# Kernel optimization log

Hardware: AMD Instinct MI355X
Metric: run time of the kernel (lower is better)

Reference implementation:

```python
import jax, jax.numpy as jnp
import numpy as np

N = 50000
E_RAND = 800000
F_IN = 256
F_OUT = 256
ALPHA = 0.2  # LeakyReLU negative slope


def setup_inputs() -> dict:
    key = jax.random.key(0)
    k1, k2, k3, k4 = jax.random.split(key, 4)
    x = jax.random.normal(k1, (N, F_IN), dtype=jnp.float32)
    # random edges + self-loops so every row has at least one edge (avoids div by 0)
    edge_rand = jax.random.randint(k2, (2, E_RAND), 0, N)
    loops = jnp.arange(N)
    edge = jnp.concatenate([edge_rand, jnp.stack([loops, loops])], axis=1)  # [2, 850000]
    W = jax.random.normal(k3, (F_IN, F_OUT), dtype=jnp.float32) * 0.05
    a = jax.random.normal(k4, (2 * F_OUT,), dtype=jnp.float32) * 0.05
    return {"x": x, "edge": edge, "W": W, "a": a}


def reference(x, edge, W, a):
    # x: [N, F_in], edge: [2, E] (row = dst/aggregation index per torch.sparse.mm(a, h))
    n = x.shape[0]
    f_out = W.shape[1]
    h = x @ W  # [N, F_out]
    src, dst = edge[0], edge[1]
    # a @ [h_src; h_dst] decomposes into two per-node dot products (no [E, 2F] concat)
    s = h @ a[:f_out]   # [N]
    t = h @ a[f_out:]   # [N]
    logit = s[src] + t[dst]                                  # [E]
    e = jnp.exp(-jax.nn.leaky_relu(logit, ALPHA))            # [E]
    rowsum = jax.ops.segment_sum(e, src, num_segments=n)     # [N]
    msg = e[:, None] * h[dst]                                # [E, F_out]
    h_prime = jax.ops.segment_sum(msg, src, num_segments=n)  # [N, F_out]
    h_prime = h_prime / rowsum[:, None]
    return jax.nn.relu(h_prime)  # concat=True path
```

## Files before the change

### kernel.cpp

```cpp
#include <hip/hip_runtime.h>
#include <hip/hip_fp16.h>

#define FDIM 256
#define ALPHA 0.2f

typedef _Float16 half8 __attribute__((ext_vector_type(8)));
typedef _Float16 half4 __attribute__((ext_vector_type(4)));
typedef float floatx4 __attribute__((ext_vector_type(4)));

__global__ __launch_bounds__(256) void prep_hist(const float* __restrict__ W,
                                                 _Float16* __restrict__ wswz,
                                                 const int* __restrict__ edge,
                                                 int* __restrict__ deg, int E) {
  if (blockIdx.x < 32) {
    const int g = blockIdx.x * 256 + threadIdx.x;
    const int kc = g >> 11, L = g & 2047;
    const int n = L >> 3, c = L & 7;
    half8 hv;
#pragma unroll
    for (int j = 0; j < 8; ++j)
      hv[j] = (_Float16)W[(size_t)(kc * 64 + c * 8 + j) * 256 + n];
    *(half8*)(wswz + (size_t)g * 8) = hv;
  } else {
    const int e = (blockIdx.x - 32) * 256 + threadIdx.x;
    if (e < E) atomicAdd(&deg[edge[e]], 1);
  }
}

#define HT_STRIDE 264
__global__ __launch_bounds__(256) void gemm_mfma(
    const float* __restrict__ x, const _Float16* __restrict__ wswz,
    const float* __restrict__ a, _Float16* __restrict__ h,
    float* __restrict__ s, float* __restrict__ t, int M) {
  __shared__ __align__(16) _Float16 smem[64 * HT_STRIDE];
  _Float16* As = smem;
  const int tid = threadIdx.x;
  const int w = tid >> 6, l = tid & 63;
  const int l15 = l & 15, q = l >> 4;
  const int row0 = blockIdx.x * 64;

  floatx4 acc[4][4];
#pragma unroll
  for (int mt = 0; mt < 4; ++mt)
#pragma unroll
    for (int nt = 0; nt < 4; ++nt) acc[mt][nt] = (floatx4){0.f, 0.f, 0.f, 0.f};

  const int id0 = tid, id1 = 256 + tid;
  const int m0 = id0 >> 3, c0 = (id0 & 7) ^ (m0 & 7);
  const int m1 = id1 >> 3, c1 = (id1 & 7) ^ (m1 & 7);
  const int r0 = row0 + m0, r1 = row0 + m1;

  float4 pf[2][2];
  auto loadA = [&](int kc) {
    pf[0][0] = pf[0][1] = pf[1][0] = pf[1][1] = make_float4(0.f, 0.f, 0.f, 0.f);
    if (r0 < M) {
      const float4* p = (const float4*)(x + (size_t)r0 * 256 + kc * 64 + c0 * 8);
      pf[0][0] = p[0];
      pf[0][1] = p[1];
    }
    if (r1 < M) {
      const float4* p = (const float4*)(x + (size_t)r1 * 256 + kc * 64 + c1 * 8);
      pf[1][0] = p[0];
      pf[1][1] = p[1];
    }
  };
  auto storeA = [&]() {
#pragma unroll
    for (int hf = 0; hf < 2; ++hf) {
      half8 hv;
      hv[0] = (_Float16)pf[hf][0].x; hv[1] = (_Float16)pf[hf][0].y;
      hv[2] = (_Float16)pf[hf][0].z; hv[3] = (_Float16)pf[hf][0].w;
      hv[4] = (_Float16)pf[hf][1].x; hv[5] = (_Float16)pf[hf][1].y;
      hv[6] = (_Float16)pf[hf][1].z; hv[7] = (_Float16)pf[hf][1].w;
      *(half8*)(As + (size_t)(hf * 256 + tid) * 8) = hv;
    }
  };

  loadA(0);
  for (int kc = 0; kc < 4; ++kc) {
    storeA();
    half8 bf[2][4];
#pragma unroll
    for (int ks = 0; ks < 2; ++ks) {
      const int c = ks * 4 + q;
#pragma unroll
      for (int nt = 0; nt < 4; ++nt) {
        const int n = w * 64 + nt * 16 + l15;
        bf[ks][nt] = *(const half8*)(wswz + (size_t)(kc * 2048 + n * 8 + c) * 8);
      }
    }
    __syncthreads();
    if (kc < 3) loadA(kc + 1);
#pragma unroll
    for (int ks = 0; ks < 2; ++ks) {
      const int c = ks * 4 + q;
      half8 af[4];
#pragma unroll
      for (int mt = 0; mt < 4; ++mt) {
        const int m = mt * 16 + l15;
        af[mt] = *(const half8*)(As + (size_t)(m * 8 + (c ^ (m & 7))) * 8);
      }
#pragma unroll
      for (int mt = 0; mt < 4; ++mt)
#pragma unroll
        for (int nt = 0; nt < 4; ++nt)
          acc[mt][nt] = __builtin_amdgcn_mfma_f32_16x16x32_f16(
              af[mt], bf[ks][nt], acc[mt][nt], 0, 0, 0);
    }
    __syncthreads();
  }

#pragma unroll
  for (int mt = 0; mt < 4; ++mt)
#pragma unroll
    for (int nt = 0; nt < 4; ++nt)
#pragma unroll
      for (int r = 0; r < 4; ++r)
        smem[(size_t)(mt * 16 + q * 4 + r) * HT_STRIDE + w * 64 + nt * 16 +
             l15] = (_Float16)acc[mt][nt][r];
  __syncthreads();

  const int w8 = tid >> 5;
  const int colh = (tid & 31) * 8;
#pragma unroll
  for (int p = 0; p < 8; ++p) {
    const int rl = p * 8 + w8;
    const int row = row0 + rl;
    if (row < M)
      *(half8*)(h + (size_t)row * 256 + colh) =
          *(const half8*)(smem + (size_t)rl * HT_STRIDE + colh);
  }

  const int r8 = tid >> 2, seg = tid & 3;
  float sp = 0.f, tp = 0.f;
#pragma unroll
  for (int c8 = 0; c8 < 8; ++c8) {
    const int col = seg * 64 + c8 * 8;
    const half8 hv = *(const half8*)(smem + (size_t)r8 * HT_STRIDE + col);
    const float4 a0 = *(const float4*)(a + col);
    const float4 a1 = *(const float4*)(a + col + 4);
    const float4 b0 = *(const float4*)(a + 256 + col);
    const float4 b1 = *(const float4*)(a + 256 + col + 4);
    sp += (float)hv[0] * a0.x + (float)hv[1] * a0.y + (float)hv[2] * a0.z +
          (float)hv[3] * a0.w + (float)hv[4] * a1.x + (float)hv[5] * a1.y +
          (float)hv[6] * a1.z + (float)hv[7] * a1.w;
    tp += (float)hv[0] * b0.x + (float)hv[1] * b0.y + (float)hv[2] * b0.z +
          (float)hv[3] * b0.w + (float)hv[4] * b1.x + (float)hv[5] * b1.y +
          (float)hv[6] * b1.z + (float)hv[7] * b1.w;
  }
  sp += __shfl_xor(sp, 1);
  sp += __shfl_xor(sp, 2);
  tp += __shfl_xor(tp, 1);
  tp += __shfl_xor(tp, 2);
  if (seg == 0 && row0 + r8 < M) {
    s[row0 + r8] = sp;
    t[row0 + r8] = tp;
  }
}

__global__ __launch_bounds__(1024) void scan1(const int* __restrict__ deg,
                                              int* __restrict__ rowstart,
                                              int* __restrict__ bsum, int n) {
  const int tid = threadIdx.x;
  const int i = blockIdx.x * 1024 + tid;
  const int val = (i < n) ? deg[i] : 0;
  const int lane = tid & 63, wv = tid >> 6;
  int v = val;
#pragma unroll
  for (int off = 1; off < 64; off <<= 1) {
    const int o = __shfl_up(v, off);
    if (lane >= off) v += o;
  }
  __shared__ int wsum[16];
  __shared__ int woff[16];
  if (lane == 63) wsum[wv] = v;
  __syncthreads();
  if (tid < 16) {
    int wv2 = wsum[tid];
#pragma unroll
    for (int off = 1; off < 16; off <<= 1) {
      const int o = __shfl_up(wv2, off);
      if (tid >= off) wv2 += o;
    }
    woff[tid] = wv2;
  }
  __syncthreads();
  const int incl = v + (wv ? woff[wv - 1] : 0);
  if (i < n) rowstart[i] = incl - val;
  if (tid == 1023) bsum[blockIdx.x] = woff[15];
}

__global__ __launch_bounds__(64) void scan2(const int* __restrict__ bsum,
                                            int* __restrict__ boff,
                                            int* __restrict__ rowstart, int nb,
                                            int n) {
  const int tid = threadIdx.x;
  int v = (tid < nb) ? bsum[tid] : 0;
#pragma unroll
  for (int off = 1; off < 64; off <<= 1) {
    const int o = __shfl_up(v, off);
    if (tid >= off) v += o;
  }
  if (tid < nb) boff[tid] = v;
  if (tid == nb - 1) rowstart[n] = v;
}

__global__ __launch_bounds__(1024) void scan3(int* __restrict__ rowstart,
                                              const int* __restrict__ boff,
                                              int n) {
  const int i = blockIdx.x * 1024 + threadIdx.x;
  if (i < n && blockIdx.x > 0) rowstart[i] += boff[blockIdx.x - 1];
}

__global__ void scatter_kernel(const int* __restrict__ edge,
                               const int* __restrict__ rowstart,
                               int* __restrict__ cursor,
                               const float* __restrict__ s,
                               const float* __restrict__ t,
                               int2* __restrict__ sde, int E) {
  const int e = blockIdx.x * 256 + threadIdx.x;
  if (e < E) {
    const int src = edge[e];
    const int dst = edge[E + e];
    const float logit = s[src] + t[dst];
    const float lr = logit > 0.f ? logit : ALPHA * logit;
    const float ev = __expf(-lr);
    const int p = atomicAdd(&cursor[src], 1);
    sde[rowstart[src] + p] = make_int2(dst, __float_as_int(ev));
  }
}

__global__ __launch_bounds__(256) void agg_kernel(
    const __half* __restrict__ h, const int* __restrict__ rowstart,
    const int2* __restrict__ sde, float* __restrict__ out, int n) {
  const int w = threadIdx.x >> 6, l = threadIdx.x & 63;
  const int row = blockIdx.x * 4 + w;
  if (row >= n) return;
  const int start = rowstart[row], end = rowstart[row + 1];
  const size_t fo = (size_t)l * 4;
  float a0 = 0.f, a1 = 0.f, a2 = 0.f, a3 = 0.f, rs = 0.f;
  int j = start;
  for (; j + 3 < end; j += 4) {
    const int2 p0 = sde[j], p1 = sde[j + 1], p2 = sde[j + 2], p3 = sde[j + 3];
    const half4 v0 = *(const half4*)(h + (size_t)p0.x * 256 + fo);
    const half4 v1 = *(const half4*)(h + (size_t)p1.x * 256 + fo);
    const half4 v2 = *(const half4*)(h + (size_t)p2.x * 256 + fo);
    const half4 v3 = *(const half4*)(h + (size_t)p3.x * 256 + fo);
    const float e0 = __int_as_float(p0.y), e1 = __int_as_float(p1.y);
    const float e2 = __int_as_float(p2.y), e3 = __int_as_float(p3.y);
    rs += (e0 + e1) + (e2 + e3);
    a0 += e0 * (float)v0[0] + e1 * (float)v1[0] + e2 * (float)v2[0] + e3 * (float)v3[0];
    a1 += e0 * (float)v0[1] + e1 * (float)v1[1] + e2 * (float)v2[1] + e3 * (float)v3[1];
    a2 += e0 * (float)v0[2] + e1 * (float)v1[2] + e2 * (float)v2[2] + e3 * (float)v3[2];
    a3 += e0 * (float)v0[3] + e1 * (float)v1[3] + e2 * (float)v2[3] + e3 * (float)v3[3];
  }
  for (; j < end; ++j) {
    const int2 p = sde[j];
    const half4 v = *(const half4*)(h + (size_t)p.x * 256 + fo);
    const float ev = __int_as_float(p.y);
    rs += ev;
    a0 += ev * (float)v[0];
    a1 += ev * (float)v[1];
    a2 += ev * (float)v[2];
    a3 += ev * (float)v[3];
  }
  const float inv = 1.f / rs;
  float4 o;
  o.x = a0 * inv; o.y = a1 * inv; o.z = a2 * inv; o.w = a3 * inv;
  o.x = o.x > 0.f ? o.x : 0.f;
  o.y = o.y > 0.f ? o.y : 0.f;
  o.z = o.z > 0.f ? o.z : 0.f;
  o.w = o.w > 0.f ? o.w : 0.f;
  *(float4*)(out + (size_t)row * 256 + fo) = o;
}

extern "C" void kernel_launch(void* const* d_in, const int* in_sizes, int n_in,
                              void* d_out, int out_size, void* d_ws,
                              size_t ws_size, hipStream_t stream) {
  const float* x = (const float*)d_in[0];
  const int* edge = (const int*)d_in[1];
  const float* W = (const float*)d_in[2];
  const float* a = (const float*)d_in[3];
  float* out = (float*)d_out;
  const int N = in_sizes[0] / FDIM;
  const int E = in_sizes[1] / 2;
  const int NB = (N + 1023) / 1024;

  __half* h = (__half*)d_ws;
  _Float16* wswz = (_Float16*)(h + (size_t)N * FDIM);
  float* s = (float*)(wswz + 8192 * 8);
  float* t = s + N;
  int* deg = (int*)(t + N);
  int* cursor = deg + N;
  int* rowstart = cursor + N;
  int* bsum = rowstart + N + 2;
  int* boff = bsum + 64;
  int2* sde = (int2*)(boff + 64);

  hipMemsetAsync(deg, 0, (size_t)2 * N * sizeof(int), stream);

  prep_hist<<<32 + (E + 255) / 256, 256, 0, stream>>>(W, wswz, edge, deg, E);
  gemm_mfma<<<(N + 63) / 64, 256, 0, stream>>>(x, wswz, a, (_Float16*)h, s, t,
                                               N);
  scan1<<<NB, 1024, 0, stream>>>(deg, rowstart, bsum, N);
  scan2<<<1, 64, 0, stream>>>(bsum, boff, rowstart, NB, N);
  scan3<<<NB, 1024, 0, stream>>>(rowstart, boff, N);
  scatter_kernel<<<(E + 255) / 256, 256, 0, stream>>>(edge, rowstart, cursor, s,
                                                      t, sde, E);
  agg_kernel<<<(N + 3) / 4, 256, 0, stream>>>(h, rowstart, sde, out, N);
}
```

Before: 278.9 us.

## Widen aggregation gathers to 16-byte loads and fold the scatter cursor into rowstart

The aggregation kernel now splits each 64-lane wave into two halves. Each half processes alternate edges and loads 8 fp16 features per lane (16 bytes) instead of 4, and the halves are combined with a cross-half shuffle at the end. The scatter kernel now gets its write position with a single atomic on a copy of rowstart that scan3 initialises, which removes the separate cursor array, its memset, and a dependent rowstart read. The cost is a shuffle reduction per row, padding work for odd tail edges, and a different output lane mapping.

Result: faster. 272.2 us (-2.4%).

```diff
diff --git a/kernel.cpp b/kernel.cpp
--- a/kernel.cpp
+++ b/kernel.cpp
@@ -5,7 +5,6 @@
 #define ALPHA 0.2f
 
 typedef _Float16 half8 __attribute__((ext_vector_type(8)));
-typedef _Float16 half4 __attribute__((ext_vector_type(4)));
 typedef float floatx4 __attribute__((ext_vector_type(4)));
 
 __global__ __launch_bounds__(256) void prep_hist(const float* __restrict__ W,
@@ -206,15 +205,19 @@
 }
 
 __global__ __launch_bounds__(1024) void scan3(int* __restrict__ rowstart,
+                                              int* __restrict__ rsc,
                                               const int* __restrict__ boff,
                                               int n) {
   const int i = blockIdx.x * 1024 + threadIdx.x;
-  if (i < n && blockIdx.x > 0) rowstart[i] += boff[blockIdx.x - 1];
+  if (i < n) {
+    const int v = rowstart[i] + (blockIdx.x ? boff[blockIdx.x - 1] : 0);
+    rowstart[i] = v;
+    rsc[i] = v;
+  }
 }
 
 __global__ void scatter_kernel(const int* __restrict__ edge,
-                               const int* __restrict__ rowstart,
-                               int* __restrict__ cursor,
+                               int* __restrict__ rsc,
                                const float* __restrict__ s,
                                const float* __restrict__ t,
                                int2* __restrict__ sde, int E) {
@@ -225,53 +228,56 @@
     const float logit = s[src] + t[dst];
     const float lr = logit > 0.f ? logit : ALPHA * logit;
     const float ev = __expf(-lr);
-    const int p = atomicAdd(&cursor[src], 1);
-    sde[rowstart[src] + p] = make_int2(dst, __float_as_int(ev));
+    const int pos = atomicAdd(&rsc[src], 1);
+    sde[pos] = make_int2(dst, __float_as_int(ev));
   }
 }
 
 __global__ __launch_bounds__(256) void agg_kernel(
-    const __half* __restrict__ h, const int* __restrict__ rowstart,
+    const _Float16* __restrict__ h, const int* __restrict__ rowstart,
     const int2* __restrict__ sde, float* __restrict__ out, int n) {
   const int w = threadIdx.x >> 6, l = threadIdx.x & 63;
   const int row = blockIdx.x * 4 + w;
   if (row >= n) return;
   const int start = rowstart[row], end = rowstart[row + 1];
-  const size_t fo = (size_t)l * 4;
-  float a0 = 0.f, a1 = 0.f, a2 = 0.f, a3 = 0.f, rs = 0.f;
+  const int half = l >> 5;
+  const int lh = l & 31;
+  const size_t fo = (size_t)lh * 8;
+  float acc[8] = {};
+  float rs = 0.f;
   int j = start;
-  for (; j + 3 < end; j += 4) {
-    const int2 p0 = sde[j], p1 = sde[j + 1], p2 = sde[j + 2], p3 = sde[j + 3];
-    const half4 v0 = *(const half4*)(h + (size_t)p0.x * 256 + fo);
-    const half4 v1 = *(const half4*)(h + (size_t)p1.x * 256 + fo);
-    const half4 v2 = *(const half4*)(h + (size_t)p2.x * 256 + fo);
-    const half4 v3 = *(const half4*)(h + (size_t)p3.x * 256 + fo);
-    const float e0 = __int_as_float(p0.y), e1 = __int_as_float(p1.y);
-    const float e2 = __int_as_float(p2.y), e3 = __int_as_float(p3.y);
-    rs += (e0 + e1) + (e2 + e3);
-    a0 += e0 * (float)v0[0] + e1 * (float)v1[0] + e2 * (float)v2[0] + e3 * (float)v3[0];
-    a1 += e0 * (float)v0[1] + e1 * (float)v1[1] + e2 * (float)v2[1] + e3 * (float)v3[1];
-    a2 += e0 * (float)v0[2] + e1 * (float)v1[2] + e2 * (float)v2[2] + e3 * (float)v3[2];
-    a3 += e0 * (float)v0[3] + e1 * (float)v1[3] + e2 * (float)v2[3] + e3 * (float)v3[3];
-  }
-  for (; j < end; ++j) {
-    const int2 p = sde[j];
-    const half4 v = *(const half4*)(h + (size_t)p.x * 256 + fo);
-    const float ev = __int_as_float(p.y);
-    rs += ev;
-    a0 += ev * (float)v[0];
-    a1 += ev * (float)v[1];
-    a2 += ev * (float)v[2];
-    a3 += ev * (float)v[3];
-  }
+  for (; j + 8 <= end; j += 8) {
+#pragma unroll
+    for (int u = 0; u < 4; ++u) {
+      const int2 p = sde[j + u * 2 + half];
+      const half8 v = *(const half8*)(h + (size_t)p.x * 256 + fo);
+      const float e = __int_as_float(p.y);
+      rs += e;
+#pragma unroll
+      for (int k = 0; k < 8; ++k) acc[k] += e * (float)v[k];
+    }
+  }
+  for (; j < end; j += 2) {
+    const int idx = j + half;
+    const bool valid = idx < end;
+    const int2 p = valid ? sde[idx] : make_int2(0, 0);
+    const half8 v = *(const half8*)(h + (size_t)p.x * 256 + fo);
+    const float e = valid ? __int_as_float(p.y) : 0.f;
+    rs += e;
+#pragma unroll
+    for (int k = 0; k < 8; ++k) acc[k] += e * (float)v[k];
+  }
+  rs += __shfl_xor(rs, 32);
+#pragma unroll
+  for (int k = 0; k < 8; ++k) acc[k] += __shfl_xor(acc[k], 32);
   const float inv = 1.f / rs;
   float4 o;
-  o.x = a0 * inv; o.y = a1 * inv; o.z = a2 * inv; o.w = a3 * inv;
-  o.x = o.x > 0.f ? o.x : 0.f;
-  o.y = o.y > 0.f ? o.y : 0.f;
-  o.z = o.z > 0.f ? o.z : 0.f;
-  o.w = o.w > 0.f ? o.w : 0.f;
-  *(float4*)(out + (size_t)row * 256 + fo) = o;
+#pragma unroll
+  for (int k = 0; k < 4; ++k) {
+    const float vv = acc[half * 4 + k] * inv;
+    (&o.x)[k] = vv > 0.f ? vv : 0.f;
+  }
+  *(float4*)(out + (size_t)row * 256 + lh * 8 + half * 4) = o;
 }
 
 extern "C" void kernel_launch(void* const* d_in, const int* in_sizes, int n_in,
@@ -286,26 +292,24 @@
   const int E = in_sizes[1] / 2;
   const int NB = (N + 1023) / 1024;
 
-  __half* h = (__half*)d_ws;
-  _Float16* wswz = (_Float16*)(h + (size_t)N * FDIM);
+  _Float16* h = (_Float16*)d_ws;
+  _Float16* wswz = h + (size_t)N * FDIM;
   float* s = (float*)(wswz + 8192 * 8);
   float* t = s + N;
   int* deg = (int*)(t + N);
-  int* cursor = deg + N;
-  int* rowstart = cursor + N;
+  int* rsc = deg + N;
+  int* rowstart = rsc + N;
   int* bsum = rowstart + N + 2;
   int* boff = bsum + 64;
   int2* sde = (int2*)(boff + 64);
 
-  hipMemsetAsync(deg, 0, (size_t)2 * N * sizeof(int), stream);
+  hipMemsetAsync(deg, 0, (size_t)N * sizeof(int), stream);
 
   prep_hist<<<32 + (E + 255) / 256, 256, 0, stream>>>(W, wswz, edge, deg, E);
-  gemm_mfma<<<(N + 63) / 64, 256, 0, stream>>>(x, wswz, a, (_Float16*)h, s, t,
-                                               N);
+  gemm_mfma<<<(N + 63) / 64, 256, 0, stream>>>(x, wswz, a, h, s, t, N);
   scan1<<<NB, 1024, 0, stream>>>(deg, rowstart, bsum, N);
   scan2<<<1, 64, 0, stream>>>(bsum, boff, rowstart, NB, N);
-  scan3<<<NB, 1024, 0, stream>>>(rowstart, boff, N);
-  scatter_kernel<<<(E + 255) / 256, 256, 0, stream>>>(edge, rowstart, cursor, s,
-                                                      t, sde, E);
+  scan3<<<NB, 1024, 0, stream>>>(rowstart, rsc, boff, N);
+  scatter_kernel<<<(E + 255) / 256, 256, 0, stream>>>(edge, rsc, s, t, sde, E);
   agg_kernel<<<(N + 3) / 4, 256, 0, stream>>>(h, rowstart, sde, out, N);
 }
```
